# Kernel optimization log

Measured on AMD Instinct MI355X. Metric: run time of the kernel, lower is better.

The kernel has to match this reference:

```python
import jax, jax.numpy as jnp
import numpy as np

B, S, T, L, D, H = 32, 64, 256, 8, 128, 128
SIGNAL_SD = 1.0 - 0.001   # default signal_sds init
NOISE_SD = 0.01           # GP diagonal jitter (noise_sds) for Cholesky stability


def setup_inputs() -> dict:
    key = jax.random.key(0)
    ks = jax.random.split(key, 8)
    X = jax.random.normal(ks[0], (B, T, D), dtype=jnp.float32)
    times = (jnp.arange(T, dtype=jnp.float32) / T) * 10.0  # span [0, 10)
    log_taus = jax.random.normal(ks[1], (L,), dtype=jnp.float32) * 0.1 + jnp.log(0.5)
    log_R_diag = jax.random.normal(ks[2], (D,), dtype=jnp.float32) * 0.1
    W1 = jax.random.normal(ks[3], (L, H), dtype=jnp.float32) / np.sqrt(L)
    b1 = jnp.zeros((H,), dtype=jnp.float32)
    W2 = jax.random.normal(ks[4], (H, D), dtype=jnp.float32) / np.sqrt(H)
    b2 = jnp.zeros((D,), dtype=jnp.float32)
    eps = jax.random.normal(ks[5], (B, S, L, T), dtype=jnp.float32)
    return {"X": X, "times": times, "log_taus": log_taus, "log_R_diag": log_R_diag,
            "W1": W1, "b1": b1, "W2": W2, "b2": b2, "eps": eps}


def reference(X, times, log_taus, log_R_diag, W1, b1, W2, b2, eps):
    taus = jnp.exp(log_taus)            # [L]
    r = jnp.exp(log_R_diag)             # [D] diagonal of R

    # --- GP prior kernel matrices (squared-exponential SDE kernel), one per latent dim ---
    dt = times[:, None] - times[None, :]                       # [T,T]
    K = (SIGNAL_SD ** 2) * jnp.exp(-(dt ** 2)[None] / (2.0 * (taus ** 2)[:, None, None]))
    K = K + (NOISE_SD ** 2) * jnp.eye(T, dtype=K.dtype)        # [L,T,T]
    Lc = jnp.linalg.cholesky(K)                                # [L,T,T]

    # --- reparameterized prior samples: z = Lc @ eps ---
    z = jnp.einsum('lut,bslt->bslu', Lc, eps)                  # [B,S,L,T]
    Z = jnp.transpose(z, (0, 1, 3, 2))                         # [B,S,T,L]

    # --- decoder MLP: latent -> manifold mean in observation space ---
    h = jnp.tanh(jnp.einsum('bstl,lh->bsth', Z, W1) + b1)      # [B,S,T,H]
    mu = jnp.einsum('bsth,hd->bstd', h, W2) + b2               # [B,S,T,D]

    # --- diagonal-R Gaussian log_prob per timestep, closed form ---
    diff = X[:, None, :, :] - mu                               # [B,S,T,D]
    quad = jnp.sum(diff * diff / r, axis=-1)                   # [B,S,T]
    log_norm = 0.5 * (jnp.sum(log_R_diag) + D * jnp.log(2.0 * jnp.pi))
    logp = -0.5 * quad - log_norm                              # [B,S,T]

    # --- sum over time, logsumexp over MC samples ---
    ll = jnp.sum(logp, axis=2)                                 # [B,S]
    nll = -(jax.scipy.special.logsumexp(ll, axis=1) - jnp.log(jnp.float32(S)))
    return nll                                                 # [B]
```

## Files before the change

kernel.cpp:

```cpp
#include <hip/hip_runtime.h>
#include <hip/hip_bf16.h>
#include <math.h>

#define B_ 32
#define S_ 64
#define T_ 256
#define L_ 8
#define D_ 128
#define H_ 128

typedef __attribute__((ext_vector_type(8))) short short8;
typedef __attribute__((ext_vector_type(4))) short short4v;
typedef __attribute__((ext_vector_type(4))) float float4v;
typedef __attribute__((ext_vector_type(4))) int int4v;

__device__ __forceinline__ short f2bf(float x) {
  __hip_bfloat16 h = __float2bfloat16(x);
  return *reinterpret_cast<short*>(&h);
}

__device__ __forceinline__ float rdlane(float x, int sl) {
  return __int_as_float(__builtin_amdgcn_readlane(__float_as_int(x), sl));
}
__device__ __forceinline__ float dpp_shr1(float x, float tailv) {
  int r = __builtin_amdgcn_update_dpp(__float_as_int(tailv), __float_as_int(x),
                                      0x138, 0xF, 0xF, false);
  return __int_as_float(r);
}

__global__ __launch_bounds__(64) void k_chol_prep(
    const float* __restrict__ times, const float* __restrict__ log_taus,
    __hip_bfloat16* __restrict__ Lcbf_,
    const float* __restrict__ W1, const float* __restrict__ W2,
    __hip_bfloat16* __restrict__ W1T, __hip_bfloat16* __restrict__ W2T,
    const float* __restrict__ eps, __hip_bfloat16* __restrict__ Eg)
{
  __shared__ short panel[256][68];
  const int bi = blockIdx.x;
  const int j = threadIdx.x;

  if (bi >= 72) {
    short* EgS = (short*)Eg;
    const int e = bi - 72;
    const int sub = j >> 3, part = j & 7;
#pragma unroll 1
    for (int p = 0; p < 16; ++p) {
      const int ri = e * 128 + p * 8 + sub;
      const int l = ri & 7, bs = ri >> 3;
      const float* src = eps + (size_t)ri * 256;
      short* dst = EgS + ((size_t)(l << 11) + bs) * 256;
#pragma unroll
      for (int g = 0; g < 8; ++g) {
        const int c = (part + g * 8) * 4;
        float4v f = *(const float4v*)(src + c);
        short4v o;
#pragma unroll
        for (int jj = 0; jj < 4; ++jj) o[jj] = f2bf(f[jj]);
        *(short4v*)&dst[c] = o;
      }
    }
    return;
  }

  if (bi >= 8) {
    const int base = (bi - 8) * 64 + j;
    for (int idx = base; idx < H_ * D_; idx += 4096) {
      const int cc = idx >> 7, h = idx & 127;
      const int n = cc & 15, nt = cc >> 4;
      const int d = n * 8 + nt;
      W2T[(size_t)cc * H_ + h] = __float2bfloat16(W2[(size_t)h * D_ + d]);
    }
    for (int idx = base; idx < L_ * H_; idx += 4096) {
      const int li = idx >> 7, h = idx & 127;
      const int msrc = 32 * (h >> 5) + 2 * (h & 15) + ((h >> 4) & 1);
      W1T[(size_t)h * L_ + li] = __float2bfloat16(W1[(size_t)li * H_ + msrc]);
    }
    return;
  }

  const int l = bi;
  short* Lbf = (short*)Lcbf_ + (size_t)l * T_ * T_;

  const float tau = expf(log_taus[l]);
  const float inv2tau2 = 0.5f / (tau * tau);
  const float sig2 = 0.999f * 0.999f;
  const float t0 = times[0];

  const float c0 = sig2 + 1e-4f;
  const float isc0 = 1.0f / sqrtf(c0);

  float u[4], v[4];
#pragma unroll
  for (int c = 0; c < 4; ++c) {
    const int d = c * 64 + j;
    const float dt = times[d] - t0;
    float cv = sig2 * __expf(-dt * dt * inv2tau2);
    if (d == 0) cv = c0;
    u[c] = cv * isc0;
    v[c] = (d == 0) ? 0.0f : u[c];
  }

#pragma unroll
  for (int p = 0; p < 4; ++p) {
    for (int kk = 0; kk < 64; ++kk) {
      const float uk = rdlane(u[p], kk);
      const float vk = rdlane(v[p], kk);
      const float dd = fmaxf(__builtin_fmaf(uk, uk, -vk * vk), 1e-20f);
      const float rr = __builtin_amdgcn_rsqf(dd);
      const float s = uk * rr;
      const float sr = vk * rr;

      float up[4];
#pragma unroll
      for (int c = 0; c < 4; ++c) {
        if (c >= p) {
          const float uc = u[c], vc = v[c];
          up[c] = s * uc - sr * vc;
          v[c]  = s * vc - sr * uc;
          const float val = (c > p || j >= kk) ? up[c] : 0.0f;
          panel[(c - p) * 64 + j][kk] = f2bf(val);
        }
      }
#pragma unroll
      for (int c = 3; c >= 0; --c) {
        if (c >= p) {
          const float tail = (c > p) ? rdlane(up[c - 1], 63) : 0.0f;
          u[c] = dpp_shr1(up[c], tail);
        }
      }
    }
    __syncthreads();
    const int rpt = 256 - 64 * p;
    const int rsub = j >> 4, cp = (j & 15) * 4;
    for (int i0 = 0; i0 < rpt; i0 += 4) {
      const int pr = i0 + rsub;
      short4v vv = *(const short4v*)&panel[pr][cp];
      *(short4v*)&Lbf[((size_t)(p * 64 + pr) << 8) + p * 64 + cp] = vv;
    }
    __syncthreads();
  }
}

__global__ __launch_bounds__(256) void k_zgemm(
    const float* __restrict__ eps, const __hip_bfloat16* __restrict__ Eg,
    const __hip_bfloat16* __restrict__ Lcbf_,
    __hip_bfloat16* __restrict__ Zg, const int useEg)
{
  __shared__ __align__(16) short E[32][264];
  const int bi = blockIdx.x;
  const int l = bi & 7, bs0 = (bi >> 3) * 32;
  const int tid = threadIdx.x, w = tid >> 6, lane = tid & 63;
  const int n = lane & 15, q = lane >> 4;
  const short* Lb = (const short*)Lcbf_ + (size_t)l * T_ * T_;

  if (!useEg) {
    const int row = tid >> 3, part = tid & 7;
    const float* src = eps + ((size_t)(bs0 + row) * L_ + l) * T_;
#pragma unroll
    for (int g = 0; g < 8; ++g) {
      const int c = (part + g * 8) * 4;
      float4v f = *(const float4v*)(src + c);
      short4v o;
#pragma unroll
      for (int jj = 0; jj < 4; ++jj) o[jj] = f2bf(f[jj]);
      *(short4v*)&E[row][c] = o;
    }
    __syncthreads();
  }

  float4v acc[4][2];
#pragma unroll
  for (int mi = 0; mi < 4; ++mi)
#pragma unroll
    for (int nt = 0; nt < 2; ++nt) acc[mi][nt] = (float4v){0.f, 0.f, 0.f, 0.f};

  const int kmax = ((15 - w + 2) >> 1) << 5;
  if (useEg) {
    const short* Eb = (const short*)Eg + ((size_t)(l << 11) + bs0) * 256;
    for (int k0 = 0; k0 < kmax; k0 += 32) {
      short8 bfrg[2];
#pragma unroll
      for (int nt = 0; nt < 2; ++nt)
        bfrg[nt] = *(const short8*)&Eb[(size_t)(nt * 16 + n) * 256 + k0 + q * 8];
#pragma unroll
      for (int mi = 0; mi < 4; ++mi) {
        const int tile = (mi == 0) ? w : (mi == 1) ? (15 - w) : (mi == 2) ? (7 - w) : (8 + w);
        const int kc = ((tile + 2) >> 1) << 5;
        if (k0 < kc) {
          const int u = tile * 16 + n;
          const short8 afr = *(const short8*)&Lb[((size_t)u << 8) + k0 + q * 8];
#pragma unroll
          for (int nt = 0; nt < 2; ++nt)
            acc[mi][nt] = __builtin_amdgcn_mfma_f32_16x16x32_bf16(afr, bfrg[nt], acc[mi][nt], 0, 0, 0);
        }
      }
    }
  } else {
    for (int k0 = 0; k0 < kmax; k0 += 32) {
      short8 bfrg[2];
#pragma unroll
      for (int nt = 0; nt < 2; ++nt)
        bfrg[nt] = *(const short8*)&E[nt * 16 + n][k0 + q * 8];
#pragma unroll
      for (int mi = 0; mi < 4; ++mi) {
        const int tile = (mi == 0) ? w : (mi == 1) ? (15 - w) : (mi == 2) ? (7 - w) : (8 + w);
        const int kc = ((tile + 2) >> 1) << 5;
        if (k0 < kc) {
          const int u = tile * 16 + n;
          const short8 afr = *(const short8*)&Lb[((size_t)u << 8) + k0 + q * 8];
#pragma unroll
          for (int nt = 0; nt < 2; ++nt)
            acc[mi][nt] = __builtin_amdgcn_mfma_f32_16x16x32_bf16(afr, bfrg[nt], acc[mi][nt], 0, 0, 0);
        }
      }
    }
  }
  __syncthreads();

#pragma unroll
  for (int mi = 0; mi < 4; ++mi) {
    const int tile = (mi == 0) ? w : (mi == 1) ? (15 - w) : (mi == 2) ? (7 - w) : (8 + w);
#pragma unroll
    for (int nt = 0; nt < 2; ++nt) {
      short4v o;
#pragma unroll
      for (int r = 0; r < 4; ++r) o[r] = f2bf(acc[mi][nt][r]);
      *(short4v*)&E[nt * 16 + n][tile * 16 + q * 4] = o;
    }
  }
  __syncthreads();

  {
    const int row = tid >> 3, part = tid & 7;
    short* dst = (short*)Zg + ((size_t)l * (B_ * S_) + bs0 + row) * T_;
#pragma unroll
    for (int g = 0; g < 4; ++g) {
      const int c = (g * 8 + part) * 8;
      *(short8*)&dst[c] = *(const short8*)&E[row][c];
    }
  }
}

__global__ __launch_bounds__(256, 4) void k_decode(
    const float* __restrict__ X, const __hip_bfloat16* __restrict__ Zg,
    const __hip_bfloat16* __restrict__ W1T, const float* __restrict__ b1,
    const __hip_bfloat16* __restrict__ W2T, const float* __restrict__ b2,
    const float* __restrict__ log_R, float* __restrict__ ll)
{
  __shared__ __align__(16) short Zt[256][8];
  __shared__ __align__(16) __hip_bfloat16 hS[32][136];
  __shared__ float redbuf[4];

  const int bid = blockIdx.x;
  const int bs = (bid & 7) * 256 + (bid >> 3);
  const int b = bs >> 6;
  const int tid = threadIdx.x;
  const int w = tid >> 6, lane = tid & 63;
  const int n = lane & 15, q = lane >> 4;
  const unsigned short* Zs = (const unsigned short*)Zg;
  const short* W1s = (const short*)W1T;
  const short* W2s = (const short*)W2T;

  {
    const size_t base = (size_t)bs * T_ + tid;
    const size_t lstr = (size_t)(B_ * S_) * T_;
    unsigned int p0 = (unsigned int)Zs[base]            | ((unsigned int)Zs[base + lstr]     << 16);
    unsigned int p1 = (unsigned int)Zs[base + 2 * lstr] | ((unsigned int)Zs[base + 3 * lstr] << 16);
    unsigned int p2 = (unsigned int)Zs[base + 4 * lstr] | ((unsigned int)Zs[base + 5 * lstr] << 16);
    unsigned int p3 = (unsigned int)Zs[base + 6 * lstr] | ((unsigned int)Zs[base + 7 * lstr] << 16);
    int4v zi = {(int)p0, (int)p1, (int)p2, (int)p3};
    *(int4v*)&Zt[tid][0] = zi;
  }

  float sLR = log_R[lane] + log_R[lane + 64];
#pragma unroll
  for (int off = 32; off >= 1; off >>= 1) sLR += __shfl_xor(sLR, off);

  const float L22 = 2.8853900817779268f;
  const int d0 = n * 8 + 2 * w;
  const int hc = 32 * w + 2 * n;
  float invr2[2], b22[2], pb[2];
#pragma unroll
  for (int jj = 0; jj < 2; ++jj) {
    invr2[jj] = expf(-log_R[d0 + jj]);
    b22[jj] = b2[d0 + jj];
    pb[jj] = b1[hc + jj] * L22;
  }

  const short8 zero8 = {0, 0, 0, 0, 0, 0, 0, 0};
  short8 w1f[2];
  short8 bfr[2][4];
#pragma unroll
  for (int jj = 0; jj < 2; ++jj) {
    const int c = (2 * w + jj) * 16 + n;
    short8 v = zero8;
    if (q == 0) v = *(const short8*)&W1s[(size_t)c * L_];
    w1f[jj] = v;
#pragma unroll
    for (int ks = 0; ks < 4; ++ks)
      bfr[jj][ks] = *(const short8*)&W2s[(size_t)c * H_ + ks * 32 + q * 8];
  }

  float qsum = 0.0f;
  __syncthreads();

#pragma unroll 1
  for (int ph = 0; ph < 8; ++ph) {
    short* hp = (short*)hS + (q * 4) * 136 + hc;
#pragma unroll 1
    for (int mi = 0; mi < 2; ++mi) {
      short8 zf = zero8;
      if (q == 0) zf = *(const short8*)&Zt[ph * 32 + mi * 16 + n][0];
      float4v c0 = __builtin_amdgcn_mfma_f32_16x16x32_bf16(zf, w1f[0], (float4v){0.f,0.f,0.f,0.f}, 0, 0, 0);
      float4v c1 = __builtin_amdgcn_mfma_f32_16x16x32_bf16(zf, w1f[1], (float4v){0.f,0.f,0.f,0.f}, 0, 0, 0);
#pragma unroll
      for (int r = 0; r < 4; ++r) {
        const float a0 = __builtin_fmaf(c0[r], L22, pb[0]);
        const float a1 = __builtin_fmaf(c1[r], L22, pb[1]);
        const float p0 = __builtin_amdgcn_exp2f(a0) + 1.f;
        const float p1 = __builtin_amdgcn_exp2f(a1) + 1.f;
        const float rj = __builtin_amdgcn_rcpf(p0 * p1);
        const float h0 = __builtin_fmaf(-2.f * p1, rj, 1.f);
        const float h1 = __builtin_fmaf(-2.f * p0, rj, 1.f);
        float2 hv2; hv2.x = h0; hv2.y = h1;
        *reinterpret_cast<__hip_bfloat162*>(hp + r * 136) = __float22bfloat162_rn(hv2);
      }
      hp += 16 * 136;
    }
    __syncthreads();
#pragma unroll 1
    for (int mi = 0; mi < 2; ++mi) {
      short8 af[4];
#pragma unroll
      for (int ks = 0; ks < 4; ++ks)
        af[ks] = *(const short8*)&hS[mi * 16 + n][ks * 32 + q * 8];
      float4v acc0 = (float4v){0.f, 0.f, 0.f, 0.f};
      float4v acc1 = (float4v){0.f, 0.f, 0.f, 0.f};
#pragma unroll
      for (int ks = 0; ks < 4; ++ks) {
        acc0 = __builtin_amdgcn_mfma_f32_16x16x32_bf16(af[ks], bfr[0][ks], acc0, 0, 0, 0);
        acc1 = __builtin_amdgcn_mfma_f32_16x16x32_bf16(af[ks], bfr[1][ks], acc1, 0, 0, 0);
      }
      const int tbase = ph * 32 + mi * 16 + q * 4;
#pragma unroll
      for (int r = 0; r < 4; ++r) {
        const int t = tbase + r;
        const float2 xv = *(const float2*)(X + (((size_t)b << 8) + t) * D_ + d0);
        float diff0 = xv.x - (acc0[r] + b22[0]);
        float diff1 = xv.y - (acc1[r] + b22[1]);
        qsum += diff0 * diff0 * invr2[0] + diff1 * diff1 * invr2[1];
      }
    }
    __syncthreads();
  }

#pragma unroll
  for (int off = 32; off >= 1; off >>= 1) qsum += __shfl_xor(qsum, off);
  if (lane == 0) redbuf[w] = qsum;
  __syncthreads();
  if (tid == 0) {
    float Q = redbuf[0] + redbuf[1] + redbuf[2] + redbuf[3];
    float log_norm = 0.5f * (sLR + (float)D_ * 1.8378770664093453f);
    ll[bs] = -0.5f * Q - (float)T_ * log_norm;
  }
}

__global__ __launch_bounds__(64) void k_lse(
    const float* __restrict__ ll, float* __restrict__ out)
{
  const int b = blockIdx.x;
  const int s = threadIdx.x;
  float v = ll[b * 64 + s];
  float m = v;
#pragma unroll
  for (int off = 32; off >= 1; off >>= 1) m = fmaxf(m, __shfl_xor(m, off));
  float e = __expf(v - m);
#pragma unroll
  for (int off = 32; off >= 1; off >>= 1) e += __shfl_xor(e, off);
  if (s == 0) out[b] = -(m + __logf(e) - 4.1588830833596715f);
}

extern "C" void kernel_launch(void* const* d_in, const int* in_sizes, int n_in,
                              void* d_out, int out_size, void* d_ws, size_t ws_size,
                              hipStream_t stream) {
  const float* X        = (const float*)d_in[0];
  const float* times    = (const float*)d_in[1];
  const float* log_taus = (const float*)d_in[2];
  const float* log_R    = (const float*)d_in[3];
  const float* W1       = (const float*)d_in[4];
  const float* b1       = (const float*)d_in[5];
  const float* W2       = (const float*)d_in[6];
  const float* b2       = (const float*)d_in[7];
  const float* eps      = (const float*)d_in[8];
  float* out = (float*)d_out;

  char* ws = (char*)d_ws;
  __hip_bfloat16* Lcbf = (__hip_bfloat16*)(ws);
  __hip_bfloat16* Zg   = (__hip_bfloat16*)(ws + 1048576);
  float* ll            = (float*)(ws + 9437184);
  __hip_bfloat16* W2T  = (__hip_bfloat16*)(ws + 9445376);
  __hip_bfloat16* W1T  = (__hip_bfloat16*)(ws + 9478144);
  __hip_bfloat16* Eg   = (__hip_bfloat16*)(ws + 9480192);

  const int useEg = (ws_size >= (size_t)9480192 + 8388608) ? 1 : 0;

  hipLaunchKernelGGL(k_chol_prep, dim3(useEg ? 200 : 72), dim3(64), 0, stream,
                     times, log_taus, Lcbf, W1, W2, W1T, W2T, eps, Eg);
  hipLaunchKernelGGL(k_zgemm,     dim3(512),  dim3(256), 0, stream, eps, Eg, Lcbf, Zg, useEg);
  hipLaunchKernelGGL(k_decode,    dim3(2048), dim3(256), 0, stream, X, Zg, W1T, b1, W2T, b2, log_R, ll);
  hipLaunchKernelGGL(k_lse,       dim3(32),   dim3(64),  0, stream, ll, out);
}
```

Before: 155.1 us.

## Block Cholesky pivot computation, split eps conversion wider, two samples per decode block

The Cholesky sweep now precomputes eight rotation coefficients per block of columns from readlane'd pivots. This shortens the serial dependency chain of readlane, rsq and update per column. The eps-to-bf16 conversion is spread over four times as many blocks, each doing less work, to raise parallelism in the prep kernel. The decode kernel now processes two (b,s) samples per block with half the grid, which amortizes the W1/W2 fragment loads and setup, at the cost of fewer blocks and a serialized second pass.

```diff
diff --git a/kernel.cpp b/kernel.cpp
--- a/kernel.cpp
+++ b/kernel.cpp
@@ -44,8 +44,8 @@
     const int e = bi - 72;
     const int sub = j >> 3, part = j & 7;
 #pragma unroll 1
-    for (int p = 0; p < 16; ++p) {
-      const int ri = e * 128 + p * 8 + sub;
+    for (int p = 0; p < 4; ++p) {
+      const int ri = e * 32 + p * 8 + sub;
       const int l = ri & 7, bs = ri >> 3;
       const float* src = eps + (size_t)ri * 256;
       short* dst = EgS + ((size_t)(l << 11) + bs) * 256;
@@ -102,30 +102,57 @@
 
 #pragma unroll
   for (int p = 0; p < 4; ++p) {
-    for (int kk = 0; kk < 64; ++kk) {
-      const float uk = rdlane(u[p], kk);
-      const float vk = rdlane(v[p], kk);
-      const float dd = fmaxf(__builtin_fmaf(uk, uk, -vk * vk), 1e-20f);
-      const float rr = __builtin_amdgcn_rsqf(dd);
-      const float s = uk * rr;
-      const float sr = vk * rr;
-
-      float up[4];
-#pragma unroll
-      for (int c = 0; c < 4; ++c) {
-        if (c >= p) {
-          const float uc = u[c], vc = v[c];
-          up[c] = s * uc - sr * vc;
-          v[c]  = s * vc - sr * uc;
-          const float val = (c > p || j >= kk) ? up[c] : 0.0f;
-          panel[(c - p) * 64 + j][kk] = f2bf(val);
-        }
-      }
-#pragma unroll
-      for (int c = 3; c >= 0; --c) {
-        if (c >= p) {
-          const float tail = (c > p) ? rdlane(up[c - 1], 63) : 0.0f;
-          u[c] = dpp_shr1(up[c], tail);
+    for (int base = 0; base < 64; base += 8) {
+      float au[8], av[8];
+#pragma unroll
+      for (int t = 0; t < 8; ++t) {
+        au[t] = rdlane(u[p], base + t);
+        av[t] = rdlane(v[p], base + t);
+      }
+      float s[8], sr[8];
+#pragma unroll
+      for (int m = 0; m < 8; ++m) {
+        const float a0 = au[0], b0 = av[0];
+        const float dd = fmaxf(__builtin_fmaf(a0, a0, -b0 * b0), 1e-20f);
+        const float rr = __builtin_amdgcn_rsqf(dd);
+        s[m] = a0 * rr;
+        sr[m] = b0 * rr;
+        if (m < 7) {
+          float nu[7], nv[7];
+#pragma unroll
+          for (int t = 0; t < 7; ++t) {
+            if (t < 7 - m) {
+              nu[t] = s[m] * au[t] - sr[m] * av[t];
+              nv[t] = s[m] * av[t + 1] - sr[m] * au[t + 1];
+            }
+          }
+#pragma unroll
+          for (int t = 0; t < 7; ++t) {
+            if (t < 7 - m) { au[t] = nu[t]; av[t] = nv[t]; }
+          }
+        }
+      }
+
+#pragma unroll
+      for (int m = 0; m < 8; ++m) {
+        const int kk = base + m;
+        float A[4];
+#pragma unroll
+        for (int c = 0; c < 4; ++c) {
+          if (c >= p) {
+            const float uc = u[c], vc = v[c];
+            A[c] = s[m] * uc - sr[m] * vc;
+            v[c] = s[m] * vc - sr[m] * uc;
+            const float val = (c > p || j >= kk) ? A[c] : 0.0f;
+            panel[(c - p) * 64 + j][kk] = f2bf(val);
+          }
+        }
+#pragma unroll
+        for (int c = 3; c >= 0; --c) {
+          if (c >= p) {
+            const float tail = (c > p) ? rdlane(A[c - 1], 63) : 0.0f;
+            u[c] = dpp_shr1(A[c], tail);
+          }
         }
       }
     }
@@ -252,8 +279,8 @@
   __shared__ float redbuf[4];
 
   const int bid = blockIdx.x;
-  const int bs = (bid & 7) * 256 + (bid >> 3);
-  const int b = bs >> 6;
+  const int pair = (bid & 7) * 128 + (bid >> 3);
+  const int b = pair >> 5;
   const int tid = threadIdx.x;
   const int w = tid >> 6, lane = tid & 63;
   const int n = lane & 15, q = lane >> 4;
@@ -261,17 +288,6 @@
   const short* W1s = (const short*)W1T;
   const short* W2s = (const short*)W2T;
 
-  {
-    const size_t base = (size_t)bs * T_ + tid;
-    const size_t lstr = (size_t)(B_ * S_) * T_;
-    unsigned int p0 = (unsigned int)Zs[base]            | ((unsigned int)Zs[base + lstr]     << 16);
-    unsigned int p1 = (unsigned int)Zs[base + 2 * lstr] | ((unsigned int)Zs[base + 3 * lstr] << 16);
-    unsigned int p2 = (unsigned int)Zs[base + 4 * lstr] | ((unsigned int)Zs[base + 5 * lstr] << 16);
-    unsigned int p3 = (unsigned int)Zs[base + 6 * lstr] | ((unsigned int)Zs[base + 7 * lstr] << 16);
-    int4v zi = {(int)p0, (int)p1, (int)p2, (int)p3};
-    *(int4v*)&Zt[tid][0] = zi;
-  }
-
   float sLR = log_R[lane] + log_R[lane + 64];
 #pragma unroll
   for (int off = 32; off >= 1; off >>= 1) sLR += __shfl_xor(sLR, off);
@@ -301,67 +317,84 @@
       bfr[jj][ks] = *(const short8*)&W2s[(size_t)c * H_ + ks * 32 + q * 8];
   }
 
-  float qsum = 0.0f;
-  __syncthreads();
+  const float log_norm = 0.5f * (sLR + (float)D_ * 1.8378770664093453f);
 
 #pragma unroll 1
-  for (int ph = 0; ph < 8; ++ph) {
-    short* hp = (short*)hS + (q * 4) * 136 + hc;
+  for (int bsi = 0; bsi < 2; ++bsi) {
+    const int bs = pair * 2 + bsi;
+
+    {
+      const size_t base = (size_t)bs * T_ + tid;
+      const size_t lstr = (size_t)(B_ * S_) * T_;
+      unsigned int p0 = (unsigned int)Zs[base]            | ((unsigned int)Zs[base + lstr]     << 16);
+      unsigned int p1 = (unsigned int)Zs[base + 2 * lstr] | ((unsigned int)Zs[base + 3 * lstr] << 16);
+      unsigned int p2 = (unsigned int)Zs[base + 4 * lstr] | ((unsigned int)Zs[base + 5 * lstr] << 16);
+      unsigned int p3 = (unsigned int)Zs[base + 6 * lstr] | ((unsigned int)Zs[base + 7 * lstr] << 16);
+      int4v zi = {(int)p0, (int)p1, (int)p2, (int)p3};
+      *(int4v*)&Zt[tid][0] = zi;
+    }
+
+    float qsum = 0.0f;
+    __syncthreads();
+
 #pragma unroll 1
-    for (int mi = 0; mi < 2; ++mi) {
-      short8 zf = zero8;
-      if (q == 0) zf = *(const short8*)&Zt[ph * 32 + mi * 16 + n][0];
-      float4v c0 = __builtin_amdgcn_mfma_f32_16x16x32_bf16(zf, w1f[0], (float4v){0.f,0.f,0.f,0.f}, 0, 0, 0);
-      float4v c1 = __builtin_amdgcn_mfma_f32_16x16x32_bf16(zf, w1f[1], (float4v){0.f,0.f,0.f,0.f}, 0, 0, 0);
-#pragma unroll
-      for (int r = 0; r < 4; ++r) {
-        const float a0 = __builtin_fmaf(c0[r], L22, pb[0]);
-        const float a1 = __builtin_fmaf(c1[r], L22, pb[1]);
-        const float p0 = __builtin_amdgcn_exp2f(a0) + 1.f;
-        const float p1 = __builtin_amdgcn_exp2f(a1) + 1.f;
-        const float rj = __builtin_amdgcn_rcpf(p0 * p1);
-        const float h0 = __builtin_fmaf(-2.f * p1, rj, 1.f);
-        const float h1 = __builtin_fmaf(-2.f * p0, rj, 1.f);
-        float2 hv2; hv2.x = h0; hv2.y = h1;
-        *reinterpret_cast<__hip_bfloat162*>(hp + r * 136) = __float22bfloat162_rn(hv2);
-      }
-      hp += 16 * 136;
-    }
+    for (int ph = 0; ph < 8; ++ph) {
+      short* hp = (short*)hS + (q * 4) * 136 + hc;
+#pragma unroll 1
+      for (int mi = 0; mi < 2; ++mi) {
+        short8 zf = zero8;
+        if (q == 0) zf = *(const short8*)&Zt[ph * 32 + mi * 16 + n][0];
+        float4v c0 = __builtin_amdgcn_mfma_f32_16x16x32_bf16(zf, w1f[0], (float4v){0.f,0.f,0.f,0.f}, 0, 0, 0);
+        float4v c1 = __builtin_amdgcn_mfma_f32_16x16x32_bf16(zf, w1f[1], (float4v){0.f,0.f,0.f,0.f}, 0, 0, 0);
+#pragma unroll
+        for (int r = 0; r < 4; ++r) {
+          const float a0 = __builtin_fmaf(c0[r], L22, pb[0]);
+          const float a1 = __builtin_fmaf(c1[r], L22, pb[1]);
+          const float p0 = __builtin_amdgcn_exp2f(a0) + 1.f;
+          const float p1 = __builtin_amdgcn_exp2f(a1) + 1.f;
+          const float rj = __builtin_amdgcn_rcpf(p0 * p1);
+          const float h0 = __builtin_fmaf(-2.f * p1, rj, 1.f);
+          const float h1 = __builtin_fmaf(-2.f * p0, rj, 1.f);
+          float2 hv2; hv2.x = h0; hv2.y = h1;
+          *reinterpret_cast<__hip_bfloat162*>(hp + r * 136) = __float22bfloat162_rn(hv2);
+        }
+        hp += 16 * 136;
+      }
+      __syncthreads();
+#pragma unroll 1
+      for (int mi = 0; mi < 2; ++mi) {
+        short8 af[4];
+#pragma unroll
+        for (int ks = 0; ks < 4; ++ks)
+          af[ks] = *(const short8*)&hS[mi * 16 + n][ks * 32 + q * 8];
+        float4v acc0 = (float4v){0.f, 0.f, 0.f, 0.f};
+        float4v acc1 = (float4v){0.f, 0.f, 0.f, 0.f};
+#pragma unroll
+        for (int ks = 0; ks < 4; ++ks) {
+          acc0 = __builtin_amdgcn_mfma_f32_16x16x32_bf16(af[ks], bfr[0][ks], acc0, 0, 0, 0);
+          acc1 = __builtin_amdgcn_mfma_f32_16x16x32_bf16(af[ks], bfr[1][ks], acc1, 0, 0, 0);
+        }
+        const int tbase = ph * 32 + mi * 16 + q * 4;
+#pragma unroll
+        for (int r = 0; r < 4; ++r) {
+          const int t = tbase + r;
+          const float2 xv = *(const float2*)(X + (((size_t)b << 8) + t) * D_ + d0);
+          float diff0 = xv.x - (acc0[r] + b22[0]);
+          float diff1 = xv.y - (acc1[r] + b22[1]);
+          qsum += diff0 * diff0 * invr2[0] + diff1 * diff1 * invr2[1];
+        }
+      }
+      __syncthreads();
+    }
+
+#pragma unroll
+    for (int off = 32; off >= 1; off >>= 1) qsum += __shfl_xor(qsum, off);
+    if (lane == 0) redbuf[w] = qsum;
     __syncthreads();
-#pragma unroll 1
-    for (int mi = 0; mi < 2; ++mi) {
-      short8 af[4];
-#pragma unroll
-      for (int ks = 0; ks < 4; ++ks)
-        af[ks] = *(const short8*)&hS[mi * 16 + n][ks * 32 + q * 8];
-      float4v acc0 = (float4v){0.f, 0.f, 0.f, 0.f};
-      float4v acc1 = (float4v){0.f, 0.f, 0.f, 0.f};
-#pragma unroll
-      for (int ks = 0; ks < 4; ++ks) {
-        acc0 = __builtin_amdgcn_mfma_f32_16x16x32_bf16(af[ks], bfr[0][ks], acc0, 0, 0, 0);
-        acc1 = __builtin_amdgcn_mfma_f32_16x16x32_bf16(af[ks], bfr[1][ks], acc1, 0, 0, 0);
-      }
-      const int tbase = ph * 32 + mi * 16 + q * 4;
-#pragma unroll
-      for (int r = 0; r < 4; ++r) {
-        const int t = tbase + r;
-        const float2 xv = *(const float2*)(X + (((size_t)b << 8) + t) * D_ + d0);
-        float diff0 = xv.x - (acc0[r] + b22[0]);
-        float diff1 = xv.y - (acc1[r] + b22[1]);
-        qsum += diff0 * diff0 * invr2[0] + diff1 * diff1 * invr2[1];
-      }
-    }
-    __syncthreads();
-  }
-
-#pragma unroll
-  for (int off = 32; off >= 1; off >>= 1) qsum += __shfl_xor(qsum, off);
-  if (lane == 0) redbuf[w] = qsum;
-  __syncthreads();
-  if (tid == 0) {
-    float Q = redbuf[0] + redbuf[1] + redbuf[2] + redbuf[3];
-    float log_norm = 0.5f * (sLR + (float)D_ * 1.8378770664093453f);
-    ll[bs] = -0.5f * Q - (float)T_ * log_norm;
+    if (tid == 0) {
+      const float Q = redbuf[0] + redbuf[1] + redbuf[2] + redbuf[3];
+      ll[bs] = -0.5f * Q - (float)T_ * log_norm;
+    }
   }
 }
 
@@ -404,9 +437,9 @@
 
   const int useEg = (ws_size >= (size_t)9480192 + 8388608) ? 1 : 0;
 
-  hipLaunchKernelGGL(k_chol_prep, dim3(useEg ? 200 : 72), dim3(64), 0, stream,
+  hipLaunchKernelGGL(k_chol_prep, dim3(useEg ? 584 : 72), dim3(64), 0, stream,
                      times, log_taus, Lcbf, W1, W2, W1T, W2T, eps, Eg);
   hipLaunchKernelGGL(k_zgemm,     dim3(512),  dim3(256), 0, stream, eps, Eg, Lcbf, Zg, useEg);
-  hipLaunchKernelGGL(k_decode,    dim3(2048), dim3(256), 0, stream, X, Zg, W1T, b1, W2T, b2, log_R, ll);
+  hipLaunchKernelGGL(k_decode,    dim3(1024), dim3(256), 0, stream, X, Zg, W1T, b1, W2T, b2, log_R, ll);
   hipLaunchKernelGGL(k_lse,       dim3(32),   dim3(64),  0, stream, ll, out);
 }
```

Result: slower. 158.8 us (+2.3%).
